# Performance work log

Measured on AMD Instinct MI355X. Metric: run time of the kernel, lower is better.

Reference implementation:

```python
import jax, jax.numpy as jnp
import numpy as np

B, S, HID = 1, 2048, 1024
H, HKV, D = 16, 4, 64
THETA = 10000.0


def _rope_tables(seq_len, head_dim):
    # Matches RotaryEmbedding: emb = cat(freqs, freqs); kernel reads cos/sin at even
    # positions d for each rotated pair (d, d+1), i.e. columns 0::2 of the table.
    inv_freq = 1.0 / (THETA ** (jnp.arange(0, head_dim, 2, dtype=jnp.float32) / head_dim))
    freqs = jnp.arange(seq_len, dtype=jnp.float32)[:, None] * inv_freq[None, :]  # [S, D/2]
    emb = jnp.concatenate([freqs, freqs], axis=-1)  # [S, D]
    return jnp.cos(emb)[:, 0::2], jnp.sin(emb)[:, 0::2]  # each [S, D/2]


def _apply_rope(x, cos, sin):
    # x: [B, H, S, D]; rotate interleaved pairs (2i, 2i+1) as in the kernel.
    xe, xo = x[..., 0::2], x[..., 1::2]
    re = xe * cos - xo * sin
    ro = xe * sin + xo * cos
    return jnp.stack([re, ro], axis=-1).reshape(x.shape)


def setup_inputs() -> dict:
    key = jax.random.key(0)
    k0, k1, k2, k3, k4 = jax.random.split(key, 5)
    return {
        "hidden_states": jax.random.normal(k0, (B, S, HID), dtype=jnp.float32),
        "Wq": jax.random.normal(k1, (HID, H * D), dtype=jnp.float32) * 0.02,
        "Wk": jax.random.normal(k2, (HID, HKV * D), dtype=jnp.float32) * 0.02,
        "Wv": jax.random.normal(k3, (HID, HKV * D), dtype=jnp.float32) * 0.02,
        "Wo": jax.random.normal(k4, (H * D, HID), dtype=jnp.float32) * 0.02,
    }


def reference(hidden_states, Wq, Wk, Wv, Wo):
    b, s, _ = hidden_states.shape
    q = (hidden_states @ Wq).reshape(b, s, H, D).transpose(0, 2, 1, 3)    # [B,H,S,D]
    k = (hidden_states @ Wk).reshape(b, s, HKV, D).transpose(0, 2, 1, 3)  # [B,Hkv,S,D]
    v = (hidden_states @ Wv).reshape(b, s, HKV, D).transpose(0, 2, 1, 3)

    cos, sin = _rope_tables(s, D)
    q = _apply_rope(q, cos, sin)
    k = _apply_rope(k, cos, sin)

    G = H // HKV  # GQA group size: query head h -> kv head h // G
    qg = q.reshape(b, HKV, G, s, D)
    scale = jnp.float32(D) ** -0.5
    scores = jnp.einsum("bkgqd,bkpd->bkgqp", qg, k) * scale  # [B,Hkv,G,S,S]
    causal = jnp.tril(jnp.ones((s, s), dtype=bool))
    scores = jnp.where(causal, scores, jnp.float32(-1e30))
    probs = jax.nn.softmax(scores, axis=-1)
    out = jnp.einsum("bkgqp,bkpd->bkgqd", probs, v).reshape(b, H, s, D)
    out = out.transpose(0, 2, 1, 3).reshape(b, s, H * D)
    return out @ Wo
```

## Files before the change

### kernel.cpp

```cpp
#include <hip/hip_runtime.h>
#include <hip/hip_bf16.h>
#include <math.h>

#define SEQ   2048
#define HID   1024
#define NH    16
#define NKV   4
#define DH    64
#define GQ    (NH / NKV)
#define NQKV  1536
#define KT    64
#define QB    32
#define CH    512
#define NCH   (SEQ / CH)
#define PSTR  72
#define LNSC  0.2878231366f
#define GS    528
#define BUFS  (8 * GS)
#define QSCALE 0.18033688011112042f

typedef __attribute__((ext_vector_type(8))) short bf16x8;
typedef __attribute__((ext_vector_type(4))) float f32x4;
typedef unsigned short u16;
typedef unsigned int u32;

__device__ __forceinline__ u16 f2bf(float f) {
    union { float f; unsigned u; } x; x.f = f;
    unsigned r = x.u + 0x7fffu + ((x.u >> 16) & 1u);
    return (u16)(r >> 16);
}
__device__ __forceinline__ u32 cvtpk(float lo, float hi) {
    u32 r;
    asm("v_cvt_pk_bf16_f32 %0, %1, %2" : "=v"(r) : "v"(lo), "v"(hi));
    return r;
}
__device__ __forceinline__ void load_lds16(const u16* g, u16* l) {
    __builtin_amdgcn_global_load_lds(
        (const __attribute__((address_space(1))) unsigned int*)g,
        (__attribute__((address_space(3))) unsigned int*)l, 16, 0, 0);
}

__global__ __launch_bounds__(256) void setup(const float* __restrict__ X,
                                             const float* __restrict__ Wq,
                                             const float* __restrict__ Wk,
                                             const float* __restrict__ Wv,
                                             const float* __restrict__ Wo,
                                             u16* __restrict__ Xb,
                                             u16* __restrict__ Wt,
                                             u16* __restrict__ WoT) {
    const int z = blockIdx.z;
    if (z == 4) {
        const int idx = ((int)blockIdx.y * 64 + (int)blockIdx.x) * 256 + threadIdx.x;
        const float4 v = ((const float4*)X)[idx];
        ushort4 o;
        o.x = f2bf(v.x); o.y = f2bf(v.y); o.z = f2bf(v.z); o.w = f2bf(v.w);
        ((ushort4*)Xb)[idx] = o;
        return;
    }
    const float* in; u16* out; int N;
    if (z == 0)      { in = Wq; out = Wt;                             N = HID; }
    else if (z == 1) { in = Wk; out = Wt + (size_t)HID * HID;         N = 256; }
    else if (z == 2) { in = Wv; out = Wt + (size_t)(HID + 256) * HID; N = 256; }
    else             { in = Wo; out = WoT;                            N = HID; }

    const int n0 = blockIdx.x * 32;
    if (n0 >= N) return;
    const int k0 = blockIdx.y * 32;

    __shared__ float t[32][33];
    const int tx = threadIdx.x & 31;
    const int ty = threadIdx.x >> 5;
    #pragma unroll
    for (int i = 0; i < 4; ++i)
        t[ty + i * 8][tx] = in[(size_t)(k0 + ty + i * 8) * N + n0 + tx];
    __syncthreads();
    #pragma unroll
    for (int i = 0; i < 4; ++i)
        out[(size_t)(n0 + ty + i * 8) * HID + k0 + tx] = f2bf(t[tx][ty + i * 8]);
}

__global__ __launch_bounds__(256) void gemm_qkv(const u16* __restrict__ A,
                                                const u16* __restrict__ Bt,
                                                u16* __restrict__ Qb,
                                                u16* __restrict__ Kb,
                                                u16* __restrict__ VTg) {
    __shared__ u16 Bs[2 * BUFS];

    const int tid  = threadIdx.x;
    const int lane = tid & 63;
    const int w    = tid >> 6;
    const int c    = lane & 15;
    const int quad = lane >> 4;
    const int m0   = blockIdx.y * 64;
    const int n0   = blockIdx.x * 64;

    const u16* gB0 = Bt + (size_t)(n0 + w * 16 + (lane >> 3)) * HID + (lane & 7) * 8;
    const u16* gB1 = gB0 + (size_t)8 * HID;
    const int  gofs0 = (w * 2) * GS, gofs1 = (w * 2 + 1) * GS;

    const u16* gA = A + (size_t)(m0 + w * 16 + c) * HID + quad * 8;
    const int  bfoff = (c >> 3) * GS + (c & 7) * 64 + quad * 8;

    f32x4 acc[4];
    #pragma unroll
    for (int nt = 0; nt < 4; ++nt) acc[nt] = (f32x4){0.f, 0.f, 0.f, 0.f};

    bf16x8 afc[2], afn[2];
    afc[0] = *(const bf16x8*)gA;
    afc[1] = *(const bf16x8*)(gA + 32);
    load_lds16(gB0, &Bs[gofs0]);
    load_lds16(gB1, &Bs[gofs1]);

    const int T = HID / 64;
    for (int t = 0; t < T; ++t) {
        __syncthreads();
        if (t + 1 < T) {
            const int nb = ((t + 1) & 1) * BUFS;
            load_lds16(gB0 + (t + 1) * 64, &Bs[nb + gofs0]);
            load_lds16(gB1 + (t + 1) * 64, &Bs[nb + gofs1]);
            afn[0] = *(const bf16x8*)(gA + (t + 1) * 64);
            afn[1] = *(const bf16x8*)(gA + (t + 1) * 64 + 32);
        }
        const int b = (t & 1) * BUFS;
        bf16x8 bfr[4][2];
        #pragma unroll
        for (int nt = 0; nt < 4; ++nt)
            #pragma unroll
            for (int ks = 0; ks < 2; ++ks)
                bfr[nt][ks] = *(const bf16x8*)&Bs[b + nt * (2 * GS) + ks * 32 + bfoff];
        #pragma unroll
        for (int ks = 0; ks < 2; ++ks)
            #pragma unroll
            for (int nt = 0; nt < 4; ++nt)
                acc[nt] = __builtin_amdgcn_mfma_f32_16x16x32_bf16(afc[ks], bfr[nt][ks], acc[nt], 0, 0, 0);
        afc[0] = afn[0];
        afc[1] = afn[1];
    }

    const int s0 = m0 + w * 16 + quad * 4;
    if (n0 < 1280) {
        const bool isQ = (n0 < 1024);
        #pragma unroll
        for (int nt = 0; nt < 4; ++nt) {
            const int d = nt * 16 + c;
            const float inv_freq = __expf(-(float)(d & 30) * LNSC);
            const float sgn = (d & 1) ? 1.f : -1.f;
            #pragma unroll
            for (int rg = 0; rg < 4; ++rg) {
                const float self = acc[nt][rg];
                const float partner = __shfl_xor(self, 1);
                float sn, cs;
                __sincosf((float)(s0 + rg) * inv_freq, &sn, &cs);
                float o = fmaf(partner, sgn * sn, self * cs);
                if (isQ) {
                    Qb[(size_t)(s0 + rg) * HID + n0 + d] = f2bf(o * QSCALE);
                } else {
                    const int kh = (n0 - 1024) >> 6;
                    Kb[((size_t)kh * SEQ + s0 + rg) * DH + d] = f2bf(o);
                }
            }
        }
    } else {
        const int kh = (n0 - 1280) >> 6;
        #pragma unroll
        for (int nt = 0; nt < 4; ++nt) {
            const int d = nt * 16 + c;
            ushort4 o;
            o.x = f2bf(acc[nt][0]); o.y = f2bf(acc[nt][1]);
            o.z = f2bf(acc[nt][2]); o.w = f2bf(acc[nt][3]);
            *(ushort4*)&VTg[((size_t)kh * DH + d) * SEQ + s0] = o;
        }
    }
}

__global__ __launch_bounds__(256) void gemm64(const u16* __restrict__ A,
                                              const u16* __restrict__ Bt,
                                              float* __restrict__ C,
                                              int K, int ldc) {
    __shared__ u16 Bs[2 * BUFS];

    const int tid  = threadIdx.x;
    const int lane = tid & 63;
    const int w    = tid >> 6;
    const int c    = lane & 15;
    const int quad = lane >> 4;
    const int m0   = blockIdx.y * 64;
    const int n0   = blockIdx.x * 64;

    const u16* gB0 = Bt + (size_t)(n0 + w * 16 + (lane >> 3)) * K + (lane & 7) * 8;
    const u16* gB1 = gB0 + (size_t)8 * K;
    const int  gofs0 = (w * 2) * GS, gofs1 = (w * 2 + 1) * GS;

    const u16* gA = A + (size_t)(m0 + w * 16 + c) * K + quad * 8;
    const int  bfoff = (c >> 3) * GS + (c & 7) * 64 + quad * 8;

    f32x4 acc[4];
    #pragma unroll
    for (int nt = 0; nt < 4; ++nt) acc[nt] = (f32x4){0.f, 0.f, 0.f, 0.f};

    bf16x8 afc[2], afn[2];
    afc[0] = *(const bf16x8*)gA;
    afc[1] = *(const bf16x8*)(gA + 32);
    load_lds16(gB0, &Bs[gofs0]);
    load_lds16(gB1, &Bs[gofs1]);

    const int T = K / 64;
    for (int t = 0; t < T; ++t) {
        __syncthreads();
        if (t + 1 < T) {
            const int nb = ((t + 1) & 1) * BUFS;
            load_lds16(gB0 + (t + 1) * 64, &Bs[nb + gofs0]);
            load_lds16(gB1 + (t + 1) * 64, &Bs[nb + gofs1]);
            afn[0] = *(const bf16x8*)(gA + (t + 1) * 64);
            afn[1] = *(const bf16x8*)(gA + (t + 1) * 64 + 32);
        }
        const int b = (t & 1) * BUFS;
        bf16x8 bfr[4][2];
        #pragma unroll
        for (int nt = 0; nt < 4; ++nt)
            #pragma unroll
            for (int ks = 0; ks < 2; ++ks)
                bfr[nt][ks] = *(const bf16x8*)&Bs[b + nt * (2 * GS) + ks * 32 + bfoff];
        #pragma unroll
        for (int ks = 0; ks < 2; ++ks)
            #pragma unroll
            for (int nt = 0; nt < 4; ++nt)
                acc[nt] = __builtin_amdgcn_mfma_f32_16x16x32_bf16(afc[ks], bfr[nt][ks], acc[nt], 0, 0, 0);
        afc[0] = afn[0];
        afc[1] = afn[1];
    }

    #pragma unroll
    for (int nt = 0; nt < 4; ++nt)
        #pragma unroll
        for (int rg = 0; rg < 4; ++rg)
            C[(size_t)(m0 + w * 16 + quad * 4 + rg) * ldc + n0 + nt * 16 + c] = acc[nt][rg];
}

__global__ __launch_bounds__(256) void attn_kernel(const u16* __restrict__ Qb,
                                                   const u16* __restrict__ Kb,
                                                   const u16* __restrict__ VTg,
                                                   float* __restrict__ Opart,
                                                   float* __restrict__ lpart,
                                                   u16* __restrict__ At) {
    __shared__ u16 Ks[2][64 * 64];
    __shared__ u16 Vs[2][64 * 64];
    __shared__ u16 Pst[4][QB * PSTR];

    const int tid  = threadIdx.x;
    const int lane = tid & 63;
    const int w    = tid >> 6;
    const int c    = lane & 15;
    const int quad = lane >> 4;
    const int kh   = blockIdx.y;
    const int z    = blockIdx.z;
    const int qt   = (SEQ / QB - 1) - (int)blockIdx.x;
    const int q0   = qt * QB;
    const int h    = kh * GQ + w;

    const int kstart = z * CH;
    const int klim   = q0 + QB;
    if (kstart >= klim) return;
    const int kend   = (klim < kstart + CH) ? klim : (kstart + CH);
    const int ntiles = (kend - kstart + KT - 1) / KT;

    bf16x8 qf[2][2];
    #pragma unroll
    for (int g = 0; g < 2; ++g)
        #pragma unroll
        for (int ks = 0; ks < 2; ++ks)
            qf[g][ks] = *(const bf16x8*)&Qb[(size_t)(q0 + g * 16 + c) * HID + h * DH + ks * 32 + quad * 8];

    f32x4 accO[4][2];
    #pragma unroll
    for (int nt = 0; nt < 4; ++nt)
        #pragma unroll
        for (int g = 0; g < 2; ++g)
            accO[nt][g] = (f32x4){0.f, 0.f, 0.f, 0.f};
    float l[2] = {0.f, 0.f};

    const int rr = lane >> 3;
    const int sw = ((lane & 7) ^ rr) * 8;

    #pragma unroll
    for (int gi = 0; gi < 2; ++gi) {
        const int row = w * 16 + gi * 8;
        load_lds16(Kb + ((size_t)kh * SEQ + kstart + row + rr) * DH + sw,
                   &Ks[0][row * 64]);
        load_lds16(VTg + ((size_t)kh * DH + row + rr) * SEQ + kstart + sw,
                   &Vs[0][row * 64]);
    }

    for (int t = 0; t < ntiles; ++t) {
        const int kt0 = kstart + t * KT;
        __syncthreads();
        if (t + 1 < ntiles) {
            const int nk = kt0 + KT;
            const int nb = (t + 1) & 1;
            #pragma unroll
            for (int gi = 0; gi < 2; ++gi) {
                const int row = w * 16 + gi * 8;
                load_lds16(Kb + ((size_t)kh * SEQ + nk + row + rr) * DH + sw,
                           &Ks[nb][row * 64]);
                load_lds16(VTg + ((size_t)kh * DH + row + rr) * SEQ + nk + sw,
                           &Vs[nb][row * 64]);
            }
        }
        const int b = t & 1;

        f32x4 accS[4][2];
        #pragma unroll
        for (int nS = 0; nS < 4; ++nS)
            #pragma unroll
            for (int g = 0; g < 2; ++g)
                accS[nS][g] = (f32x4){0.f, 0.f, 0.f, 0.f};
        #pragma unroll
        for (int nS = 0; nS < 4; ++nS)
            #pragma unroll
            for (int ks = 0; ks < 2; ++ks) {
                const bf16x8 kf = *(const bf16x8*)
                    &Ks[b][(nS * 16 + c) * 64 + (((ks * 4 + quad) ^ (c & 7)) * 8)];
                #pragma unroll
                for (int g = 0; g < 2; ++g)
                    accS[nS][g] = __builtin_amdgcn_mfma_f32_16x16x32_bf16(kf, qf[g][ks], accS[nS][g], 0, 0, 0);
            }

        #pragma unroll
        for (int g = 0; g < 2; ++g) {
            const int q = q0 + g * 16 + c;
            const bool full = (kt0 + KT - 1 <= q0 + g * 16);
            #pragma unroll
            for (int nS = 0; nS < 4; ++nS) {
                const int key = kt0 + nS * 16 + quad * 4;
                float p0, p1, p2, p3;
                if (full) {
                    p0 = __builtin_amdgcn_exp2f(accS[nS][g][0]);
                    p1 = __builtin_amdgcn_exp2f(accS[nS][g][1]);
                    p2 = __builtin_amdgcn_exp2f(accS[nS][g][2]);
                    p3 = __builtin_amdgcn_exp2f(accS[nS][g][3]);
                } else {
                    p0 = (key + 0 <= q) ? __builtin_amdgcn_exp2f(accS[nS][g][0]) : 0.f;
                    p1 = (key + 1 <= q) ? __builtin_amdgcn_exp2f(accS[nS][g][1]) : 0.f;
                    p2 = (key + 2 <= q) ? __builtin_amdgcn_exp2f(accS[nS][g][2]) : 0.f;
                    p3 = (key + 3 <= q) ? __builtin_amdgcn_exp2f(accS[nS][g][3]) : 0.f;
                }
                l[g] += (p0 + p1) + (p2 + p3);
                u32* dst = (u32*)&Pst[w][(g * 16 + c) * PSTR + nS * 16 + quad * 4];
                dst[0] = cvtpk(p0, p1);
                dst[1] = cvtpk(p2, p3);
            }
        }
        __threadfence_block();

        #pragma unroll
        for (int ks2 = 0; ks2 < 2; ++ks2) {
            bf16x8 pf[2];
            #pragma unroll
            for (int g = 0; g < 2; ++g)
                pf[g] = *(const bf16x8*)&Pst[w][(g * 16 + c) * PSTR + ks2 * 32 + quad * 8];
            #pragma unroll
            for (int nt = 0; nt < 4; ++nt) {
                const bf16x8 vf = *(const bf16x8*)
                    &Vs[b][(nt * 16 + c) * 64 + (((ks2 * 4 + quad) ^ (c & 7)) * 8)];
                #pragma unroll
                for (int g = 0; g < 2; ++g)
                    accO[nt][g] = __builtin_amdgcn_mfma_f32_16x16x32_bf16(vf, pf[g], accO[nt][g], 0, 0, 0);
            }
        }
    }

    const int nchunks = (q0 + QB + CH - 1) / CH;

    if (nchunks == 1) {
        #pragma unroll
        for (int g = 0; g < 2; ++g) {
            float lg = l[g];
            lg += __shfl_xor(lg, 16);
            lg += __shfl_xor(lg, 32);
            const float inv = 1.0f / lg;
            u16* Ap = At + (size_t)(q0 + g * 16 + c) * HID + h * DH;
            #pragma unroll
            for (int nt = 0; nt < 4; ++nt) {
                ushort4 o;
                o.x = f2bf(accO[nt][g][0] * inv);
                o.y = f2bf(accO[nt][g][1] * inv);
                o.z = f2bf(accO[nt][g][2] * inv);
                o.w = f2bf(accO[nt][g][3] * inv);
                *(ushort4*)&Ap[nt * 16 + quad * 4] = o;
            }
        }
        return;
    }

    #pragma unroll
    for (int g = 0; g < 2; ++g) {
        float lg = l[g];
        lg += __shfl_xor(lg, 16);
        lg += __shfl_xor(lg, 32);
        if (quad == 0)
            lpart[((size_t)z * SEQ + q0 + g * 16 + c) * NH + h] = lg;

        float* Op = Opart + ((size_t)z * SEQ + q0 + g * 16 + c) * HID + h * DH;
        #pragma unroll
        for (int nt = 0; nt < 4; ++nt)
            *(f32x4*)&Op[nt * 16 + quad * 4] = accO[nt][g];
    }
}

__global__ __launch_bounds__(256) void attn_reduce(const float* __restrict__ Opart,
                                                   const float* __restrict__ lpart,
                                                   u16* __restrict__ At) {
    const int idx = blockIdx.x * 256 + threadIdx.x + (CH * HID / 4);
    const int q  = idx >> 8;
    const int h  = (idx & 255) >> 4;
    const int klim = (q & ~(QB - 1)) + QB;
    float4 o = ((const float4*)Opart)[idx];
    float  l = lpart[q * NH + h];
    #pragma unroll
    for (int z = 1; z < NCH; ++z) {
        if (z * CH < klim) {
            const float4 o1 = ((const float4*)Opart)[idx + z * (SEQ * HID / 4)];
            o.x += o1.x; o.y += o1.y; o.z += o1.z; o.w += o1.w;
            l += lpart[(z * SEQ + q) * NH + h];
        }
    }
    const float inv = 1.0f / l;
    ushort4 r;
    r.x = f2bf(o.x * inv); r.y = f2bf(o.y * inv);
    r.z = f2bf(o.z * inv); r.w = f2bf(o.w * inv);
    ((ushort4*)At)[idx] = r;
}

extern "C" void kernel_launch(void* const* d_in, const int* in_sizes, int n_in,
                              void* d_out, int out_size, void* d_ws, size_t ws_size,
                              hipStream_t stream) {
    const float* X  = (const float*)d_in[0];
    const float* Wq = (const float*)d_in[1];
    const float* Wk = (const float*)d_in[2];
    const float* Wv = (const float*)d_in[3];
    const float* Wo = (const float*)d_in[4];
    float* out = (float*)d_out;

    u16* Wt     = (u16*)d_ws;
    u16* WoT    = Wt + (size_t)NQKV * HID;
    u16* Xb     = WoT + (size_t)HID * HID;
    u16* At     = Xb + (size_t)SEQ * HID;
    u16* Qb     = At + (size_t)SEQ * HID;
    u16* Kb     = Qb + (size_t)SEQ * HID;
    u16* VTg    = Kb + (size_t)NKV * SEQ * DH;
    float* Opart = (float*)(VTg + (size_t)NKV * DH * SEQ);
    float* lpart = Opart + (size_t)NCH * SEQ * HID;

    dim3 blk(256);

    setup<<<dim3(64, 32, 5), blk, 0, stream>>>(X, Wq, Wk, Wv, Wo, Xb, Wt, WoT);

    gemm_qkv<<<dim3(NQKV / 64, SEQ / 64), blk, 0, stream>>>(Xb, Wt, Qb, Kb, VTg);

    attn_kernel<<<dim3(SEQ / QB, NKV, NCH), blk, 0, stream>>>(Qb, Kb, VTg, Opart, lpart, At);

    attn_reduce<<<((SEQ - CH) * HID / 4) / 256, blk, 0, stream>>>(Opart, lpart, At);

    gemm64<<<dim3(HID / 64, SEQ / 64), blk, 0, stream>>>(At, WoT, out, HID, HID);
}
```

Baseline: 131.4 us.

## Load K/V fragments directly from global into registers, drop LDS staging and barriers

```diff
diff --git a/kernel.cpp b/kernel.cpp
--- a/kernel.cpp
+++ b/kernel.cpp
@@ -243,8 +243,6 @@
                                                    float* __restrict__ Opart,
                                                    float* __restrict__ lpart,
                                                    u16* __restrict__ At) {
-    __shared__ u16 Ks[2][64 * 64];
-    __shared__ u16 Vs[2][64 * 64];
     __shared__ u16 Pst[4][QB * PSTR];
 
     const int tid  = threadIdx.x;
@@ -279,34 +277,25 @@
             accO[nt][g] = (f32x4){0.f, 0.f, 0.f, 0.f};
     float l[2] = {0.f, 0.f};
 
-    const int rr = lane >> 3;
-    const int sw = ((lane & 7) ^ rr) * 8;
-
-    #pragma unroll
-    for (int gi = 0; gi < 2; ++gi) {
-        const int row = w * 16 + gi * 8;
-        load_lds16(Kb + ((size_t)kh * SEQ + kstart + row + rr) * DH + sw,
-                   &Ks[0][row * 64]);
-        load_lds16(VTg + ((size_t)kh * DH + row + rr) * SEQ + kstart + sw,
-                   &Vs[0][row * 64]);
-    }
+    const u16* Kbase = Kb + ((size_t)kh * SEQ + c) * DH + quad * 8;
+    const u16* Vbase = VTg + ((size_t)kh * DH + c) * SEQ + quad * 8;
 
     for (int t = 0; t < ntiles; ++t) {
         const int kt0 = kstart + t * KT;
-        __syncthreads();
-        if (t + 1 < ntiles) {
-            const int nk = kt0 + KT;
-            const int nb = (t + 1) & 1;
-            #pragma unroll
-            for (int gi = 0; gi < 2; ++gi) {
-                const int row = w * 16 + gi * 8;
-                load_lds16(Kb + ((size_t)kh * SEQ + nk + row + rr) * DH + sw,
-                           &Ks[nb][row * 64]);
-                load_lds16(VTg + ((size_t)kh * DH + row + rr) * SEQ + nk + sw,
-                           &Vs[nb][row * 64]);
-            }
-        }
-        const int b = t & 1;
+
+        bf16x8 kf[4][2];
+        #pragma unroll
+        for (int nS = 0; nS < 4; ++nS)
+            #pragma unroll
+            for (int ks = 0; ks < 2; ++ks)
+                kf[nS][ks] = *(const bf16x8*)(Kbase + (size_t)(kt0 + nS * 16) * DH + ks * 32);
+
+        bf16x8 vf[2][4];
+        #pragma unroll
+        for (int ks2 = 0; ks2 < 2; ++ks2)
+            #pragma unroll
+            for (int nt = 0; nt < 4; ++nt)
+                vf[ks2][nt] = *(const bf16x8*)(Vbase + (size_t)(nt * 16) * SEQ + kt0 + ks2 * 32);
 
         f32x4 accS[4][2];
         #pragma unroll
@@ -314,16 +303,16 @@
             #pragma unroll
             for (int g = 0; g < 2; ++g)
                 accS[nS][g] = (f32x4){0.f, 0.f, 0.f, 0.f};
+
+        __builtin_amdgcn_s_setprio(1);
         #pragma unroll
         for (int nS = 0; nS < 4; ++nS)
             #pragma unroll
-            for (int ks = 0; ks < 2; ++ks) {
-                const bf16x8 kf = *(const bf16x8*)
-                    &Ks[b][(nS * 16 + c) * 64 + (((ks * 4 + quad) ^ (c & 7)) * 8)];
+            for (int ks = 0; ks < 2; ++ks)
                 #pragma unroll
                 for (int g = 0; g < 2; ++g)
-                    accS[nS][g] = __builtin_amdgcn_mfma_f32_16x16x32_bf16(kf, qf[g][ks], accS[nS][g], 0, 0, 0);
-            }
+                    accS[nS][g] = __builtin_amdgcn_mfma_f32_16x16x32_bf16(kf[nS][ks], qf[g][ks], accS[nS][g], 0, 0, 0);
+        __builtin_amdgcn_s_setprio(0);
 
         #pragma unroll
         for (int g = 0; g < 2; ++g) {
@@ -350,8 +339,9 @@
                 dst[1] = cvtpk(p2, p3);
             }
         }
-        __threadfence_block();
-
+        __builtin_amdgcn_fence(__ATOMIC_ACQ_REL, "wavefront");
+
+        __builtin_amdgcn_s_setprio(1);
         #pragma unroll
         for (int ks2 = 0; ks2 < 2; ++ks2) {
             bf16x8 pf[2];
@@ -360,13 +350,12 @@
                 pf[g] = *(const bf16x8*)&Pst[w][(g * 16 + c) * PSTR + ks2 * 32 + quad * 8];
             #pragma unroll
             for (int nt = 0; nt < 4; ++nt) {
-                const bf16x8 vf = *(const bf16x8*)
-                    &Vs[b][(nt * 16 + c) * 64 + (((ks2 * 4 + quad) ^ (c & 7)) * 8)];
                 #pragma unroll
                 for (int g = 0; g < 2; ++g)
-                    accO[nt][g] = __builtin_amdgcn_mfma_f32_16x16x32_bf16(vf, pf[g], accO[nt][g], 0, 0, 0);
+                    accO[nt][g] = __builtin_amdgcn_mfma_f32_16x16x32_bf16(vf[ks2][nt], pf[g], accO[nt][g], 0, 0, 0);
             }
         }
+        __builtin_amdgcn_s_setprio(0);
     }
 
     const int nchunks = (q0 + QB + CH - 1) / CH;
```

After: 164.9 us. 25.4% more time.

## Double M-tile per block in projection GEMMs and XOR-swizzle B LDS layout

Applied to the files above, without the earlier changes.

```diff
diff --git a/kernel.cpp b/kernel.cpp
--- a/kernel.cpp
+++ b/kernel.cpp
@@ -91,23 +91,34 @@
     const int w    = tid >> 6;
     const int c    = lane & 15;
     const int quad = lane >> 4;
-    const int m0   = blockIdx.y * 64;
+    const int m0   = blockIdx.y * 128;
     const int n0   = blockIdx.x * 64;
 
-    const u16* gB0 = Bt + (size_t)(n0 + w * 16 + (lane >> 3)) * HID + (lane & 7) * 8;
+    const int rg8 = lane >> 3;
+    const u16* gB0 = Bt + (size_t)(n0 + w * 16 + rg8) * HID + (((lane & 7) ^ rg8) * 8);
     const u16* gB1 = gB0 + (size_t)8 * HID;
     const int  gofs0 = (w * 2) * GS, gofs1 = (w * 2 + 1) * GS;
 
-    const u16* gA = A + (size_t)(m0 + w * 16 + c) * HID + quad * 8;
-    const int  bfoff = (c >> 3) * GS + (c & 7) * 64 + quad * 8;
-
-    f32x4 acc[4];
-    #pragma unroll
-    for (int nt = 0; nt < 4; ++nt) acc[nt] = (f32x4){0.f, 0.f, 0.f, 0.f};
-
-    bf16x8 afc[2], afn[2];
-    afc[0] = *(const bf16x8*)gA;
-    afc[1] = *(const bf16x8*)(gA + 32);
+    const u16* gA0 = A + (size_t)(m0 + w * 32 + c) * HID + quad * 8;
+    const u16* gA1 = gA0 + (size_t)16 * HID;
+    const int bbase = (c >> 3) * GS + (c & 7) * 64;
+    int bsw[2];
+    #pragma unroll
+    for (int ks = 0; ks < 2; ++ks)
+        bsw[ks] = bbase + (((ks * 4 + quad) ^ (c & 7)) * 8);
+
+    f32x4 acc[2][4];
+    #pragma unroll
+    for (int mi = 0; mi < 2; ++mi)
+        #pragma unroll
+        for (int nt = 0; nt < 4; ++nt) acc[mi][nt] = (f32x4){0.f, 0.f, 0.f, 0.f};
+
+    bf16x8 afc[2][2], afn[2][2];
+    #pragma unroll
+    for (int ks = 0; ks < 2; ++ks) {
+        afc[0][ks] = *(const bf16x8*)(gA0 + ks * 32);
+        afc[1][ks] = *(const bf16x8*)(gA1 + ks * 32);
+    }
     load_lds16(gB0, &Bs[gofs0]);
     load_lds16(gB1, &Bs[gofs1]);
 
@@ -118,8 +129,11 @@
             const int nb = ((t + 1) & 1) * BUFS;
             load_lds16(gB0 + (t + 1) * 64, &Bs[nb + gofs0]);
             load_lds16(gB1 + (t + 1) * 64, &Bs[nb + gofs1]);
-            afn[0] = *(const bf16x8*)(gA + (t + 1) * 64);
-            afn[1] = *(const bf16x8*)(gA + (t + 1) * 64 + 32);
+            #pragma unroll
+            for (int ks = 0; ks < 2; ++ks) {
+                afn[0][ks] = *(const bf16x8*)(gA0 + (t + 1) * 64 + ks * 32);
+                afn[1][ks] = *(const bf16x8*)(gA1 + (t + 1) * 64 + ks * 32);
+            }
         }
         const int b = (t & 1) * BUFS;
         bf16x8 bfr[4][2];
@@ -127,48 +141,60 @@
         for (int nt = 0; nt < 4; ++nt)
             #pragma unroll
             for (int ks = 0; ks < 2; ++ks)
-                bfr[nt][ks] = *(const bf16x8*)&Bs[b + nt * (2 * GS) + ks * 32 + bfoff];
+                bfr[nt][ks] = *(const bf16x8*)&Bs[b + nt * (2 * GS) + bsw[ks]];
         #pragma unroll
         for (int ks = 0; ks < 2; ++ks)
             #pragma unroll
             for (int nt = 0; nt < 4; ++nt)
-                acc[nt] = __builtin_amdgcn_mfma_f32_16x16x32_bf16(afc[ks], bfr[nt][ks], acc[nt], 0, 0, 0);
-        afc[0] = afn[0];
-        afc[1] = afn[1];
-    }
-
-    const int s0 = m0 + w * 16 + quad * 4;
+                #pragma unroll
+                for (int mi = 0; mi < 2; ++mi)
+                    acc[mi][nt] = __builtin_amdgcn_mfma_f32_16x16x32_bf16(afc[mi][ks], bfr[nt][ks], acc[mi][nt], 0, 0, 0);
+        #pragma unroll
+        for (int ks = 0; ks < 2; ++ks) {
+            afc[0][ks] = afn[0][ks];
+            afc[1][ks] = afn[1][ks];
+        }
+    }
+
     if (n0 < 1280) {
         const bool isQ = (n0 < 1024);
         #pragma unroll
-        for (int nt = 0; nt < 4; ++nt) {
-            const int d = nt * 16 + c;
-            const float inv_freq = __expf(-(float)(d & 30) * LNSC);
-            const float sgn = (d & 1) ? 1.f : -1.f;
-            #pragma unroll
-            for (int rg = 0; rg < 4; ++rg) {
-                const float self = acc[nt][rg];
-                const float partner = __shfl_xor(self, 1);
-                float sn, cs;
-                __sincosf((float)(s0 + rg) * inv_freq, &sn, &cs);
-                float o = fmaf(partner, sgn * sn, self * cs);
-                if (isQ) {
-                    Qb[(size_t)(s0 + rg) * HID + n0 + d] = f2bf(o * QSCALE);
-                } else {
-                    const int kh = (n0 - 1024) >> 6;
-                    Kb[((size_t)kh * SEQ + s0 + rg) * DH + d] = f2bf(o);
+        for (int mi = 0; mi < 2; ++mi) {
+            const int s0 = m0 + w * 32 + mi * 16 + quad * 4;
+            #pragma unroll
+            for (int nt = 0; nt < 4; ++nt) {
+                const int d = nt * 16 + c;
+                const float inv_freq = __expf(-(float)(d & 30) * LNSC);
+                const float sgn = (d & 1) ? 1.f : -1.f;
+                #pragma unroll
+                for (int rg = 0; rg < 4; ++rg) {
+                    const float self = acc[mi][nt][rg];
+                    const float partner = __shfl_xor(self, 1);
+                    float sn, cs;
+                    __sincosf((float)(s0 + rg) * inv_freq, &sn, &cs);
+                    float o = fmaf(partner, sgn * sn, self * cs);
+                    if (isQ) {
+                        Qb[(size_t)(s0 + rg) * HID + n0 + d] = f2bf(o * QSCALE);
+                    } else {
+                        const int kh = (n0 - 1024) >> 6;
+                        Kb[((size_t)kh * SEQ + s0 + rg) * DH + d] = f2bf(o);
+                    }
                 }
             }
         }
     } else {
         const int kh = (n0 - 1280) >> 6;
         #pragma unroll
-        for (int nt = 0; nt < 4; ++nt) {
-            const int d = nt * 16 + c;
-            ushort4 o;
-            o.x = f2bf(acc[nt][0]); o.y = f2bf(acc[nt][1]);
-            o.z = f2bf(acc[nt][2]); o.w = f2bf(acc[nt][3]);
-            *(ushort4*)&VTg[((size_t)kh * DH + d) * SEQ + s0] = o;
+        for (int mi = 0; mi < 2; ++mi) {
+            const int s0 = m0 + w * 32 + mi * 16 + quad * 4;
+            #pragma unroll
+            for (int nt = 0; nt < 4; ++nt) {
+                const int d = nt * 16 + c;
+                ushort4 o;
+                o.x = f2bf(acc[mi][nt][0]); o.y = f2bf(acc[mi][nt][1]);
+                o.z = f2bf(acc[mi][nt][2]); o.w = f2bf(acc[mi][nt][3]);
+                *(ushort4*)&VTg[((size_t)kh * DH + d) * SEQ + s0] = o;
+            }
         }
     }
 }
@@ -184,23 +210,34 @@
     const int w    = tid >> 6;
     const int c    = lane & 15;
     const int quad = lane >> 4;
-    const int m0   = blockIdx.y * 64;
+    const int m0   = blockIdx.y * 128;
     const int n0   = blockIdx.x * 64;
 
-    const u16* gB0 = Bt + (size_t)(n0 + w * 16 + (lane >> 3)) * K + (lane & 7) * 8;
+    const int rg8 = lane >> 3;
+    const u16* gB0 = Bt + (size_t)(n0 + w * 16 + rg8) * K + (((lane & 7) ^ rg8) * 8);
     const u16* gB1 = gB0 + (size_t)8 * K;
     const int  gofs0 = (w * 2) * GS, gofs1 = (w * 2 + 1) * GS;
 
-    const u16* gA = A + (size_t)(m0 + w * 16 + c) * K + quad * 8;
-    const int  bfoff = (c >> 3) * GS + (c & 7) * 64 + quad * 8;
-
-    f32x4 acc[4];
-    #pragma unroll
-    for (int nt = 0; nt < 4; ++nt) acc[nt] = (f32x4){0.f, 0.f, 0.f, 0.f};
-
-    bf16x8 afc[2], afn[2];
-    afc[0] = *(const bf16x8*)gA;
-    afc[1] = *(const bf16x8*)(gA + 32);
+    const u16* gA0 = A + (size_t)(m0 + w * 32 + c) * K + quad * 8;
+    const u16* gA1 = gA0 + (size_t)16 * K;
+    const int bbase = (c >> 3) * GS + (c & 7) * 64;
+    int bsw[2];
+    #pragma unroll
+    for (int ks = 0; ks < 2; ++ks)
+        bsw[ks] = bbase + (((ks * 4 + quad) ^ (c & 7)) * 8);
+
+    f32x4 acc[2][4];
+    #pragma unroll
+    for (int mi = 0; mi < 2; ++mi)
+        #pragma unroll
+        for (int nt = 0; nt < 4; ++nt) acc[mi][nt] = (f32x4){0.f, 0.f, 0.f, 0.f};
+
+    bf16x8 afc[2][2], afn[2][2];
+    #pragma unroll
+    for (int ks = 0; ks < 2; ++ks) {
+        afc[0][ks] = *(const bf16x8*)(gA0 + ks * 32);
+        afc[1][ks] = *(const bf16x8*)(gA1 + ks * 32);
+    }
     load_lds16(gB0, &Bs[gofs0]);
     load_lds16(gB1, &Bs[gofs1]);
 
@@ -211,8 +248,11 @@
             const int nb = ((t + 1) & 1) * BUFS;
             load_lds16(gB0 + (t + 1) * 64, &Bs[nb + gofs0]);
             load_lds16(gB1 + (t + 1) * 64, &Bs[nb + gofs1]);
-            afn[0] = *(const bf16x8*)(gA + (t + 1) * 64);
-            afn[1] = *(const bf16x8*)(gA + (t + 1) * 64 + 32);
+            #pragma unroll
+            for (int ks = 0; ks < 2; ++ks) {
+                afn[0][ks] = *(const bf16x8*)(gA0 + (t + 1) * 64 + ks * 32);
+                afn[1][ks] = *(const bf16x8*)(gA1 + (t + 1) * 64 + ks * 32);
+            }
         }
         const int b = (t & 1) * BUFS;
         bf16x8 bfr[4][2];
@@ -220,21 +260,28 @@
         for (int nt = 0; nt < 4; ++nt)
             #pragma unroll
             for (int ks = 0; ks < 2; ++ks)
-                bfr[nt][ks] = *(const bf16x8*)&Bs[b + nt * (2 * GS) + ks * 32 + bfoff];
+                bfr[nt][ks] = *(const bf16x8*)&Bs[b + nt * (2 * GS) + bsw[ks]];
         #pragma unroll
         for (int ks = 0; ks < 2; ++ks)
             #pragma unroll
             for (int nt = 0; nt < 4; ++nt)
-                acc[nt] = __builtin_amdgcn_mfma_f32_16x16x32_bf16(afc[ks], bfr[nt][ks], acc[nt], 0, 0, 0);
-        afc[0] = afn[0];
-        afc[1] = afn[1];
-    }
-
-    #pragma unroll
-    for (int nt = 0; nt < 4; ++nt)
-        #pragma unroll
-        for (int rg = 0; rg < 4; ++rg)
-            C[(size_t)(m0 + w * 16 + quad * 4 + rg) * ldc + n0 + nt * 16 + c] = acc[nt][rg];
+                #pragma unroll
+                for (int mi = 0; mi < 2; ++mi)
+                    acc[mi][nt] = __builtin_amdgcn_mfma_f32_16x16x32_bf16(afc[mi][ks], bfr[nt][ks], acc[mi][nt], 0, 0, 0);
+        #pragma unroll
+        for (int ks = 0; ks < 2; ++ks) {
+            afc[0][ks] = afn[0][ks];
+            afc[1][ks] = afn[1][ks];
+        }
+    }
+
+    #pragma unroll
+    for (int mi = 0; mi < 2; ++mi)
+        #pragma unroll
+        for (int nt = 0; nt < 4; ++nt)
+            #pragma unroll
+            for (int rg = 0; rg < 4; ++rg)
+                C[(size_t)(m0 + w * 32 + mi * 16 + quad * 4 + rg) * ldc + n0 + nt * 16 + c] = acc[mi][nt][rg];
 }
 
 __global__ __launch_bounds__(256) void attn_kernel(const u16* __restrict__ Qb,
@@ -455,11 +502,11 @@
 
     setup<<<dim3(64, 32, 5), blk, 0, stream>>>(X, Wq, Wk, Wv, Wo, Xb, Wt, WoT);
 
-    gemm_qkv<<<dim3(NQKV / 64, SEQ / 64), blk, 0, stream>>>(Xb, Wt, Qb, Kb, VTg);
+    gemm_qkv<<<dim3(NQKV / 64, SEQ / 128), blk, 0, stream>>>(Xb, Wt, Qb, Kb, VTg);
 
     attn_kernel<<<dim3(SEQ / QB, NKV, NCH), blk, 0, stream>>>(Qb, Kb, VTg, Opart, lpart, At);
 
     attn_reduce<<<((SEQ - CH) * HID / 4) / 256, blk, 0, stream>>>(Opart, lpart, At);
 
-    gemm64<<<dim3(HID / 64, SEQ / 64), blk, 0, stream>>>(At, WoT, out, HID, HID);
-}
+    gemm64<<<dim3(HID / 64, SEQ / 128), blk, 0, stream>>>(At, WoT, out, HID, HID);
+}
```

New measurement: 139.9 us. 6.4% more time.
